# Performance work log

Measured on AMD Instinct MI355X. Metric: run time of the kernel, lower is better.

## Reference

```python
import jax, jax.numpy as jnp
import numpy as np

SEQ_LEN = 524288
TAGSET = 64
START = 62   # tag_to_ix['START_TAG']
STOP = 63    # tag_to_ix['STOP_TAG']
NEG = -10000.0


def setup_inputs() -> dict:
    key = jax.random.key(0)
    k1, k2 = jax.random.split(key)
    feats = jax.random.normal(k1, (SEQ_LEN, TAGSET), dtype=jnp.float32)
    # learned transition matrix; trans[next, prev], with START row / STOP col masked as in __init__
    trans = jax.random.normal(k2, (TAGSET, TAGSET), dtype=jnp.float32)
    trans = trans.at[START, :].set(NEG).at[:, STOP].set(NEG)
    return {"feats": feats, "trans": trans}


def reference(feats, trans):
    # Viterbi max-plus DP. forward_var fv[prev]; scores[next, prev] = fv[prev] + trans[next, prev]
    fv0 = jnp.full((TAGSET,), NEG, dtype=jnp.float32).at[START].set(0.0)

    def step(fv, feat):
        scores = fv[None, :] + trans            # [T_next, T_prev]
        bptr = jnp.argmax(scores, axis=1)        # best previous tag per next tag
        fv_new = jnp.max(scores, axis=1) + feat  # [T]
        return fv_new, bptr

    fv, bptrs = jax.lax.scan(step, fv0, feats)   # bptrs: [seq_len, T] int

    terminal = fv + trans[STOP]                  # transition to STOP
    best = jnp.argmax(terminal)
    path_score = terminal[best]

    # backtrack through backpointers (reverse scan), emitting tag at each step
    def back(tag, bp):
        return bp[tag], tag

    _, best_path = jax.lax.scan(back, best, bptrs, reverse=True)  # [seq_len] tags
    return path_score, best_path
```

## Files before the change

### kernel.cpp

```cpp
#include <hip/hip_runtime.h>
#include <hip/hip_bf16.h>

#define T_LEN 524288
#define NTAG 64
#define START_TAG 62
#define STOP_TAG 63
#define NEGV -10000.0f

#define KCH 4096
#define CL  128
#define WU  64
#define WPB 4

#define SG  64
#define NSG (KCH / SG)

typedef float v2f __attribute__((ext_vector_type(2)));

struct BlockLDS {
    float trL[NTAG * 65];
    __align__(16) float fv[WPB][2][NTAG];
};

static __device__ __forceinline__ float max3f(float a, float b, float c) {
    return fmaxf(fmaxf(a, b), c);
}
static __device__ __forceinline__ v2f mk2(float a, float b) {
    v2f r; r.x = a; r.y = b; return r;
}

union Q4 { float4 q; v2f h[2]; };

template<int MODE>
__device__ __forceinline__ void wave_run(
    int t0, int nsteps, const float* __restrict__ feats,
    const float* __restrict__ trans,
    unsigned int* __restrict__ bpg, float (*fv)[NTAG],
    const float* __restrict__ trL, int lane)
{
    v2f tr[32];
    {
        const float4* t4 = (const float4*)(trans + (size_t)lane * NTAG);
#pragma unroll
        for (int j = 0; j < 16; ++j) {
            float4 v = t4[j];
            tr[2 * j + 0] = mk2(v.x, v.y);
            tr[2 * j + 1] = mk2(v.z, v.w);
        }
    }
    const float* trrow = &trL[lane * 65];
    const float* fp = feats + (size_t)t0 * NTAG + lane;
    float fA[4], fB[4];
#pragma unroll
    for (int i = 0; i < 4; ++i) fA[i] = fp[i * NTAG];
    fp += 4 * NTAG;
    unsigned int acc = 0;
#pragma unroll 1
    for (int tt = 0; tt < nsteps; tt += 4) {
        const bool hav = (tt + 4 < nsteps);
        if (hav) {
#pragma unroll
            for (int i = 0; i < 4; ++i) fB[i] = fp[i * NTAG];
            fp += 4 * NTAG;
        }
#pragma unroll
        for (int s = 0; s < 4; ++s) {
            const int st = tt + s;
            const float* fvp = fv[st & 1];
            float* fvn = fv[(st + 1) & 1];
            const Q4* fq = (const Q4*)fvp;

            float gm[8];
#pragma unroll
            for (int g = 0; g < 8; ++g) {
                Q4 x0 = fq[2 * g + 0];
                Q4 x1 = fq[2 * g + 1];
                v2f c01 = x0.h[0] + tr[4 * g + 0];
                v2f c23 = x0.h[1] + tr[4 * g + 1];
                v2f c45 = x1.h[0] + tr[4 * g + 2];
                v2f c67 = x1.h[1] + tr[4 * g + 3];
                const float m1 = max3f(c01.x, c01.y, c23.x);
                const float m2 = max3f(c23.y, c45.x, c45.y);
                const float m3 = max3f(c67.x, c67.y, m1);
                gm[g] = fmaxf(m2, m3);
            }
            const float ga = max3f(gm[0], gm[1], gm[2]);
            const float gb = max3f(gm[3], gm[4], gm[5]);
            const float gc = max3f(gm[6], gm[7], ga);
            const float t  = fmaxf(gb, gc);
            fvn[lane] = t + fA[s];

            if (MODE == 1) {
                int g = 7;
                if (gm[6] == t) g = 6;
                if (gm[5] == t) g = 5;
                if (gm[4] == t) g = 4;
                if (gm[3] == t) g = 3;
                if (gm[2] == t) g = 2;
                if (gm[1] == t) g = 1;
                if (gm[0] == t) g = 0;
                const Q4* yq = (const Q4*)(fvp + (g << 3));
                Q4 y0 = yq[0];
                Q4 y1 = yq[1];
                const float* tb = trrow + (g << 3);
                const float e0 = y0.h[0].x + tb[0], e1 = y0.h[0].y + tb[1];
                const float e2 = y0.h[1].x + tb[2], e3 = y0.h[1].y + tb[3];
                const float e4 = y1.h[0].x + tb[4], e5 = y1.h[0].y + tb[5];
                const float e6 = y1.h[1].x + tb[6], e7 = y1.h[1].y + tb[7];
                int j = 7;
                if (e6 == t) j = 6;
                if (e5 == t) j = 5;
                if (e4 == t) j = 4;
                if (e3 == t) j = 3;
                if (e2 == t) j = 2;
                if (e1 == t) j = 1;
                if (e0 == t) j = 0;
                const int idx = (g << 3) | j;
                acc |= (unsigned int)idx << (8 * s);
                if (s == 3) {
                    bpg[((size_t)(t0 + st - 3) >> 2) * NTAG + lane] = acc;
                    acc = 0;
                }
            }
        }
        if (hav) {
#pragma unroll
            for (int i = 0; i < 4; ++i) fA[i] = fB[i];
        }
    }
}

__device__ __forceinline__ void load_trans_lds(const float* __restrict__ trans,
                                               int lane, float* trL)
{
    const float4* trow = (const float4*)(trans + (size_t)lane * NTAG);
    float* dst = trL + lane * 65;
#pragma unroll
    for (int j = 0; j < 16; ++j) {
        float4 v = trow[j];
        dst[j * 4 + 0] = v.x; dst[j * 4 + 1] = v.y;
        dst[j * 4 + 2] = v.z; dst[j * 4 + 3] = v.w;
    }
}

__global__ __launch_bounds__(256, 4) void pass1_kernel(
    const float* __restrict__ feats, const float* __restrict__ trans,
    unsigned int* __restrict__ bpg, float* __restrict__ ovl,
    float* __restrict__ bnd, unsigned char* __restrict__ maps)
{
    __shared__ BlockLDS L;
    const int lane = threadIdx.x & 63;
    const int w = threadIdx.x >> 6;
    const int k = blockIdx.x * WPB + w;
    load_trans_lds(trans, lane, L.trL);

    float (*fv)[NTAG] = L.fv[w];
    if (k == 0) {
        fv[0][lane] = (lane == START_TAG) ? 0.0f : NEGV;
    } else {
        fv[0][lane] = 0.0f;
    }
    if (k > 0) {
        wave_run<0>(k * CL - WU, WU, feats, trans, nullptr, fv, L.trL, lane);
        ovl[(size_t)k * NTAG + lane] = fv[0][lane];
    }
    wave_run<1>(k * CL, CL, feats, trans, bpg, fv, L.trL, lane);
    bnd[(size_t)(k + 1) * NTAG + lane] = fv[0][lane];

    asm volatile("s_waitcnt vmcnt(0)" ::: "memory");
    int cur = lane;
    const size_t base = ((size_t)(k * CL) >> 2) * NTAG + lane;
#pragma unroll 4
    for (int t4 = CL / 4 - 1; t4 >= 0; --t4) {
        unsigned int b4 = bpg[base + (size_t)t4 * NTAG];
#pragma unroll
        for (int j = 3; j >= 0; --j) {
            unsigned int u = __shfl(b4, cur);
            cur = (u >> (8 * j)) & 255;
        }
    }
    maps[(size_t)k * NTAG + lane] = (unsigned char)cur;
}

__global__ __launch_bounds__(1024) void finalize_part_kernel(
    const float* __restrict__ bnd, const float* __restrict__ ovl,
    float* __restrict__ pc, float* __restrict__ pe, int* __restrict__ pb)
{
    __shared__ float sc[16], se[16];
    __shared__ int sb[16];
    const int tid = threadIdx.x, w = tid >> 6, lane = tid & 63;
    const int gw = blockIdx.x * 16 + w;
    float csum = 0.f, esum = 0.f;
    int bad = 0;
    for (int k = 1 + gw; k < KCH; k += 1024) {
        float d = bnd[(size_t)k * NTAG + lane] - ovl[(size_t)k * NTAG + lane];
        float d0 = __shfl(d, 0);
        float sp = fabsf(d - d0);
#pragma unroll
        for (int o = 1; o < 64; o <<= 1) sp = fmaxf(sp, __shfl_xor(sp, o));
        csum += d0; esum += sp;
        if (!(fabsf(d0) < 1.0e7f)) bad = 1;
    }
    if (lane == 0) { sc[w] = csum; se[w] = esum; sb[w] = bad; }
    __syncthreads();
    if (tid == 0) {
        float c = 0.f, e = 0.f; int b = 0;
        for (int i = 0; i < 16; ++i) { c += sc[i]; e += se[i]; b |= sb[i]; }
        pc[blockIdx.x] = c; pe[blockIdx.x] = e; pb[blockIdx.x] = b;
    }
}

__global__ __launch_bounds__(64) void finalize_final_kernel(
    const float* __restrict__ bnd, const float* __restrict__ trans,
    const float* __restrict__ feats,
    const float* __restrict__ pc, const float* __restrict__ pe,
    const int* __restrict__ pb,
    float* __restrict__ dout, int* __restrict__ bestp)
{
    __shared__ float trL[NTAG * 65];
    __shared__ __align__(16) float fv[2][NTAG];
    const int tid = threadIdx.x;
    float c = pc[tid], e = pe[tid];
    int b = pb[tid];
#pragma unroll
    for (int o = 1; o < 64; o <<= 1) {
        c += __shfl_xor(c, o);
        e += __shfl_xor(e, o);
        b |= __shfl_xor(b, o);
    }
    if (!(e <= 1.0e4f)) b = 1;
    const float shift = -c;
    float v = (bnd[(size_t)KCH * NTAG + tid] - shift) + trans[STOP_TAG * NTAG + tid];
    int bi = tid;
#pragma unroll
    for (int o = 1; o < 64; o <<= 1) {
        float vo = __shfl_xor(v, o);
        int io = __shfl_xor(bi, o);
        if (vo > v || (vo == v && io < bi)) { v = vo; bi = io; }
    }
    if (tid == 0) { dout[0] = v; dout[T_LEN] = (float)bi; *bestp = bi; }

    if (b) {
        load_trans_lds(trans, tid, trL);
        fv[0][tid] = (tid == START_TAG) ? 0.0f : NEGV;
        wave_run<0>(0, T_LEN, feats, trans, nullptr, fv, trL, tid);
        float v2 = fv[0][tid] + trans[STOP_TAG * NTAG + tid];
        int b2 = tid;
#pragma unroll
        for (int o = 1; o < 64; o <<= 1) {
            float vo = __shfl_xor(v2, o);
            int io = __shfl_xor(b2, o);
            if (vo > v2 || (vo == v2 && io < b2)) { v2 = vo; b2 = io; }
        }
        if (tid == 0) { dout[0] = v2; dout[T_LEN] = (float)b2; *bestp = b2; }
    }
}

__global__ __launch_bounds__(64) void compose_kernel(
    const unsigned char* __restrict__ maps, unsigned char* __restrict__ smaps)
{
    const int lane = threadIdx.x, j = blockIdx.x;
    int cur = lane;
#pragma unroll 4
    for (int i = (j + 1) * SG - 1; i >= j * SG; --i) {
        int m = maps[(size_t)i * NTAG + lane];
        cur = __shfl(m, cur);
    }
    smaps[j * NTAG + lane] = (unsigned char)cur;
}

__global__ __launch_bounds__(64) void fill2_kernel(
    const unsigned char* __restrict__ maps, const unsigned char* __restrict__ smaps,
    const int* __restrict__ bestp, unsigned char* __restrict__ Eblk)
{
    const int lane = threadIdx.x, j = blockIdx.x;
    int e = *bestp;
#pragma unroll 1
    for (int jj = NSG - 1; jj > j; --jj) {
        int m = smaps[jj * NTAG + lane];
        e = __shfl(m, e);
    }
#pragma unroll 4
    for (int i = (j + 1) * SG - 1; i >= j * SG; --i) {
        if (lane == 0) Eblk[i] = (unsigned char)e;
        int m = maps[(size_t)i * NTAG + lane];
        e = __shfl(m, e);
    }
}

__global__ __launch_bounds__(64) void emit_kernel(
    const unsigned int* __restrict__ bpg, const unsigned char* __restrict__ Eblk,
    float* __restrict__ dout)
{
    const int lane = threadIdx.x, k = blockIdx.x;
    const int eblk = Eblk[k];
    int cur = lane;
    const int t0 = k * CL;
    const size_t base = ((size_t)t0 >> 2) * NTAG + lane;
#pragma unroll 4
    for (int t4 = CL / 4 - 1; t4 >= 0; --t4) {
        unsigned int b4 = bpg[base + (size_t)t4 * NTAG];
#pragma unroll
        for (int j = 3; j >= 0; --j) {
            unsigned int u = __shfl(b4, cur);
            cur = (u >> (8 * j)) & 255;
            const int t = t0 + t4 * 4 + j;
            if (t > 0 && lane == eblk) dout[t] = (float)cur;
        }
    }
}

__global__ void beacon_kernel(float* dout, float wsz) { dout[0] = wsz; }

extern "C" void kernel_launch(void* const* d_in, const int* in_sizes, int n_in,
                              void* d_out, int out_size, void* d_ws, size_t ws_size,
                              hipStream_t stream) {
    const float* feats = (const float*)d_in[0];
    const float* trans = (const float*)d_in[1];
    float* dout = (float*)d_out;
    char* ws = (char*)d_ws;

    size_t off = 0;
    auto alloc = [&](size_t bytes) -> void* {
        void* p = ws + off;
        off = (off + bytes + 255) & ~(size_t)255;
        return p;
    };
    unsigned int* bpg = (unsigned int*)alloc((size_t)(T_LEN / 4) * NTAG * 4);
    float* bnd    = (float*)alloc((size_t)(KCH + 1) * NTAG * sizeof(float));
    float* ovl    = (float*)alloc((size_t)KCH * NTAG * sizeof(float));
    unsigned char* maps  = (unsigned char*)alloc((size_t)KCH * NTAG);
    unsigned char* smaps = (unsigned char*)alloc((size_t)NSG * NTAG);
    unsigned char* Eblk  = (unsigned char*)alloc(KCH);
    int*   bestp  = (int*)alloc(sizeof(int));
    float* pc     = (float*)alloc(64 * sizeof(float));
    float* pe     = (float*)alloc(64 * sizeof(float));
    int*   pb     = (int*)alloc(64 * sizeof(int));
    const size_t NEED = off;

    if (ws_size < NEED) {
        beacon_kernel<<<1, 1, 0, stream>>>(dout, (float)ws_size);
        return;
    }

    pass1_kernel<<<KCH / WPB, 256, 0, stream>>>(feats, trans, bpg, ovl, bnd, maps);
    compose_kernel<<<NSG, 64, 0, stream>>>(maps, smaps);
    finalize_part_kernel<<<64, 1024, 0, stream>>>(bnd, ovl, pc, pe, pb);
    finalize_final_kernel<<<1, 64, 0, stream>>>(bnd, trans, feats, pc, pe, pb, dout, bestp);
    fill2_kernel<<<NSG, 64, 0, stream>>>(maps, smaps, bestp, Eblk);
    emit_kernel<<<KCH, 64, 0, stream>>>(bpg, Eblk, dout);
}
```

Baseline: 384.2 us.

## Merge compose and finalize kernels, fold fill into emit, pin transition registers

Merges the chunk-map compose kernel into the finalize-part launch as extra blocks, and folds the per-chunk entry-tag computation (fill2) into the emit kernel, so each emit block recomputes its own starting tag from the segment maps. This cuts the launch count from six to four and drops the Eblk round trip. It also adds empty asm constraints so the transition values stay in registers, and replaces per-step backpointer address arithmetic with an incrementing pointer. In exchange, each emit block now does redundant serial shuffle chains over up to 64 segment maps plus up to 63 chunk maps.

```diff
diff --git a/kernel.cpp b/kernel.cpp
--- a/kernel.cpp
+++ b/kernel.cpp
@@ -47,6 +47,9 @@
             tr[2 * j + 0] = mk2(v.x, v.y);
             tr[2 * j + 1] = mk2(v.z, v.w);
         }
+#pragma unroll
+        for (int j = 0; j < 32; ++j)
+            asm volatile("" : "+v"(tr[j]));
     }
     const float* trrow = &trL[lane * 65];
     const float* fp = feats + (size_t)t0 * NTAG + lane;
@@ -55,6 +58,7 @@
     for (int i = 0; i < 4; ++i) fA[i] = fp[i * NTAG];
     fp += 4 * NTAG;
     unsigned int acc = 0;
+    unsigned int* bp = bpg + ((size_t)t0 >> 2) * NTAG + lane;
 #pragma unroll 1
     for (int tt = 0; tt < nsteps; tt += 4) {
         const bool hav = (tt + 4 < nsteps);
@@ -118,7 +122,8 @@
                 const int idx = (g << 3) | j;
                 acc |= (unsigned int)idx << (8 * s);
                 if (s == 3) {
-                    bpg[((size_t)(t0 + st - 3) >> 2) * NTAG + lane] = acc;
+                    *bp = acc;
+                    bp += NTAG;
                     acc = 0;
                 }
             }
@@ -182,14 +187,28 @@
     maps[(size_t)k * NTAG + lane] = (unsigned char)cur;
 }
 
-__global__ __launch_bounds__(1024) void finalize_part_kernel(
+__global__ __launch_bounds__(1024) void mid_kernel(
+    const unsigned char* __restrict__ maps, unsigned char* __restrict__ smaps,
     const float* __restrict__ bnd, const float* __restrict__ ovl,
     float* __restrict__ pc, float* __restrict__ pe, int* __restrict__ pb)
 {
     __shared__ float sc[16], se[16];
     __shared__ int sb[16];
+    if (blockIdx.x < NSG) {
+        if (threadIdx.x < 64) {
+            const int lane = threadIdx.x, j = blockIdx.x;
+            int cur = lane;
+#pragma unroll 4
+            for (int i = (j + 1) * SG - 1; i >= j * SG; --i) {
+                int m = maps[(size_t)i * NTAG + lane];
+                cur = __shfl(m, cur);
+            }
+            smaps[j * NTAG + lane] = (unsigned char)cur;
+        }
+        return;
+    }
     const int tid = threadIdx.x, w = tid >> 6, lane = tid & 63;
-    const int gw = blockIdx.x * 16 + w;
+    const int gw = (blockIdx.x - NSG) * 16 + w;
     float csum = 0.f, esum = 0.f;
     int bad = 0;
     for (int k = 1 + gw; k < KCH; k += 1024) {
@@ -206,7 +225,7 @@
     if (tid == 0) {
         float c = 0.f, e = 0.f; int b = 0;
         for (int i = 0; i < 16; ++i) { c += sc[i]; e += se[i]; b |= sb[i]; }
-        pc[blockIdx.x] = c; pe[blockIdx.x] = e; pb[blockIdx.x] = b;
+        pc[blockIdx.x - NSG] = c; pe[blockIdx.x - NSG] = e; pb[blockIdx.x - NSG] = b;
     }
 }
 
@@ -256,24 +275,13 @@
     }
 }
 
-__global__ __launch_bounds__(64) void compose_kernel(
-    const unsigned char* __restrict__ maps, unsigned char* __restrict__ smaps)
-{
-    const int lane = threadIdx.x, j = blockIdx.x;
-    int cur = lane;
-#pragma unroll 4
-    for (int i = (j + 1) * SG - 1; i >= j * SG; --i) {
-        int m = maps[(size_t)i * NTAG + lane];
-        cur = __shfl(m, cur);
-    }
-    smaps[j * NTAG + lane] = (unsigned char)cur;
-}
-
-__global__ __launch_bounds__(64) void fill2_kernel(
+__global__ __launch_bounds__(64) void emit2_kernel(
     const unsigned char* __restrict__ maps, const unsigned char* __restrict__ smaps,
-    const int* __restrict__ bestp, unsigned char* __restrict__ Eblk)
-{
-    const int lane = threadIdx.x, j = blockIdx.x;
+    const int* __restrict__ bestp, const unsigned int* __restrict__ bpg,
+    float* __restrict__ dout)
+{
+    const int lane = threadIdx.x, k = blockIdx.x;
+    const int j = k >> 6;
     int e = *bestp;
 #pragma unroll 1
     for (int jj = NSG - 1; jj > j; --jj) {
@@ -281,19 +289,11 @@
         e = __shfl(m, e);
     }
 #pragma unroll 4
-    for (int i = (j + 1) * SG - 1; i >= j * SG; --i) {
-        if (lane == 0) Eblk[i] = (unsigned char)e;
+    for (int i = (j + 1) * SG - 1; i > k; --i) {
         int m = maps[(size_t)i * NTAG + lane];
         e = __shfl(m, e);
     }
-}
-
-__global__ __launch_bounds__(64) void emit_kernel(
-    const unsigned int* __restrict__ bpg, const unsigned char* __restrict__ Eblk,
-    float* __restrict__ dout)
-{
-    const int lane = threadIdx.x, k = blockIdx.x;
-    const int eblk = Eblk[k];
+    const int eblk = e;
     int cur = lane;
     const int t0 = k * CL;
     const size_t base = ((size_t)t0 >> 2) * NTAG + lane;
@@ -301,10 +301,10 @@
     for (int t4 = CL / 4 - 1; t4 >= 0; --t4) {
         unsigned int b4 = bpg[base + (size_t)t4 * NTAG];
 #pragma unroll
-        for (int j = 3; j >= 0; --j) {
+        for (int jj = 3; jj >= 0; --jj) {
             unsigned int u = __shfl(b4, cur);
-            cur = (u >> (8 * j)) & 255;
-            const int t = t0 + t4 * 4 + j;
+            cur = (u >> (8 * jj)) & 255;
+            const int t = t0 + t4 * 4 + jj;
             if (t > 0 && lane == eblk) dout[t] = (float)cur;
         }
     }
@@ -331,7 +331,6 @@
     float* ovl    = (float*)alloc((size_t)KCH * NTAG * sizeof(float));
     unsigned char* maps  = (unsigned char*)alloc((size_t)KCH * NTAG);
     unsigned char* smaps = (unsigned char*)alloc((size_t)NSG * NTAG);
-    unsigned char* Eblk  = (unsigned char*)alloc(KCH);
     int*   bestp  = (int*)alloc(sizeof(int));
     float* pc     = (float*)alloc(64 * sizeof(float));
     float* pe     = (float*)alloc(64 * sizeof(float));
@@ -344,9 +343,7 @@
     }
 
     pass1_kernel<<<KCH / WPB, 256, 0, stream>>>(feats, trans, bpg, ovl, bnd, maps);
-    compose_kernel<<<NSG, 64, 0, stream>>>(maps, smaps);
-    finalize_part_kernel<<<64, 1024, 0, stream>>>(bnd, ovl, pc, pe, pb);
+    mid_kernel<<<NSG + 64, 1024, 0, stream>>>(maps, smaps, bnd, ovl, pc, pe, pb);
     finalize_final_kernel<<<1, 64, 0, stream>>>(bnd, trans, feats, pc, pe, pb, dout, bestp);
-    fill2_kernel<<<NSG, 64, 0, stream>>>(maps, smaps, bestp, Eblk);
-    emit_kernel<<<KCH, 64, 0, stream>>>(bpg, Eblk, dout);
-}
+    emit2_kernel<<<KCH, 64, 0, stream>>>(maps, smaps, bestp, bpg, dout);
+}
```

After: 384.6 us. No clear change (+0.1%).
